# Kernel optimization log

Hardware: AMD Instinct MI355X
Metric: run time of the kernel (lower is better)

Reference implementation:

```python
import jax, jax.numpy as jnp
import numpy as np

D_MODEL = 1024
NUM_HEADS = 16
HEAD_DIM = D_MODEL // NUM_HEADS


def setup_inputs() -> dict:
    key = jax.random.key(0)
    ks = jax.random.split(key, 9)
    s = 1.0 / np.sqrt(D_MODEL)
    def lin(k):
        kw, kb = jax.random.split(k)
        W = jax.random.uniform(kw, (D_MODEL, D_MODEL), jnp.float32, -s, s)
        b = jax.random.uniform(kb, (D_MODEL,), jnp.float32, -s, s)
        return W, b
    Wq, bq = lin(ks[0])
    Wk, bk = lin(ks[1])
    Wv, bv = lin(ks[2])
    Wo, bo = lin(ks[3])
    x = jax.random.normal(ks[4], (4, 2048, D_MODEL), jnp.float32)
    return {"x": x, "Wq": Wq, "bq": bq, "Wk": Wk, "bk": bk,
            "Wv": Wv, "bv": bv, "Wo": Wo, "bo": bo}


def reference(x, Wq, bq, Wk, bk, Wv, bv, Wo, bo):
    B, S, _ = x.shape
    def heads(W, b):
        # [B,S,D] -> [B,H,S,Dh]
        return (x @ W.T + b).reshape(B, S, NUM_HEADS, HEAD_DIM).transpose(0, 2, 1, 3)
    q = heads(Wq, bq)
    k = heads(Wk, bk)
    v = heads(Wv, bv)
    scale = jnp.sqrt(jnp.float32(HEAD_DIM))
    scores = jnp.einsum('bhqd,bhkd->bhqk', q, k) / scale  # [B,H,S,S]
    attn = jax.nn.softmax(scores, axis=-1)
    ctx = jnp.einsum('bhqk,bhkd->bhqd', attn, v)
    ctx = ctx.transpose(0, 2, 1, 3).reshape(B, S, D_MODEL)
    out = ctx @ Wo.T + bo
    return out
```

## Files before the change

### kernel.cpp

```cpp
#include <hip/hip_runtime.h>
#include <hip/hip_bf16.h>

typedef __bf16 bf16;
typedef __attribute__((ext_vector_type(4))) __bf16 bf16x4;
typedef __attribute__((ext_vector_type(8))) __bf16 bf16x8;
typedef __attribute__((ext_vector_type(4))) float floatx4;

#define MFMA_16x16x32(a, b, c) __builtin_amdgcn_mfma_f32_16x16x32_bf16((a), (b), (c), 0, 0, 0)

#define SOFTMAX_SC 0.18033688011112042f

__device__ __forceinline__ void async_lds16(const bf16* g, bf16* lds) {
  __builtin_amdgcn_global_load_lds(
      (__attribute__((address_space(1))) void*)(g),
      (__attribute__((address_space(3))) void*)(lds),
      16, 0, 0);
}

__global__ __launch_bounds__(256) void cast_all_kernel(
    const float* __restrict__ x,
    const float* __restrict__ Wq, const float* __restrict__ Wk,
    const float* __restrict__ Wv, const float* __restrict__ Wo,
    bf16* __restrict__ dst)
{
  const size_t xN = (size_t)8192 * 1024;
  size_t i = ((size_t)blockIdx.x * 256 + threadIdx.x) * 8;
  const float* src;
  size_t off;
  if (i < xN) { src = x; off = i; }
  else {
    size_t j = i - xN;
    int w = (int)(j >> 20);
    off = j & (((size_t)1 << 20) - 1);
    src = (w == 0) ? Wq : (w == 1) ? Wk : (w == 2) ? Wv : Wo;
  }
  floatx4 a = *(const floatx4*)(src + off);
  floatx4 b = *(const floatx4*)(src + off + 4);
  bf16x8 r;
  r[0] = (bf16)a[0]; r[1] = (bf16)a[1]; r[2] = (bf16)a[2]; r[3] = (bf16)a[3];
  r[4] = (bf16)b[0]; r[5] = (bf16)b[1]; r[6] = (bf16)b[2]; r[7] = (bf16)b[3];
  *(bf16x8*)(dst + i) = r;
}

template <typename CT>
__device__ __forceinline__ void gemm128_async_body(
    const bf16* __restrict__ A, const bf16* __restrict__ W,
    const float* __restrict__ bias, CT* __restrict__ C)
{
  __shared__ __align__(16) bf16 As[128 * 64];
  __shared__ __align__(16) bf16 Bs[128 * 64];

  const int tid  = threadIdx.x;
  const int lane = tid & 63;
  const int wave = tid >> 6;
  const int quad = lane >> 4;
  const int l15  = lane & 15;

  const int gm0   = blockIdx.y * 128;
  const int gn0   = blockIdx.x * 128;
  const int m_off = (wave >> 1) * 64;
  const int n_off = (wave & 1) * 64;

  floatx4 acc[4][4] = {};

  const bf16* ap[4];
  const bf16* wp[4];
  #pragma unroll
  for (int i = 0; i < 4; ++i) {
    int c = i * 256 + tid;
    int srow = c >> 3;
    int ksw  = (c & 7) ^ (srow & 7);
    ap[i] = A + (size_t)(gm0 + srow) * 1024 + ksw * 8;
    wp[i] = W + (size_t)(gn0 + srow) * 1024 + ksw * 8;
  }

  for (int kt = 0; kt < 16; ++kt) {
    __syncthreads();
    #pragma unroll
    for (int i = 0; i < 4; ++i) {
      int c = i * 256 + tid;
      async_lds16(ap[i], &As[c * 8]);
      async_lds16(wp[i], &Bs[c * 8]);
      ap[i] += 64; wp[i] += 64;
    }
    __syncthreads();

    #pragma unroll
    for (int kk = 0; kk < 2; ++kk) {
      bf16x8 af[4], bfr[4];
      #pragma unroll
      for (int i = 0; i < 4; ++i) {
        int rm = m_off + i * 16 + l15;
        af[i]  = *(const bf16x8*)&As[rm * 64 + (((kk * 4 + quad) ^ (rm & 7)) * 8)];
        int rn = n_off + i * 16 + l15;
        bfr[i] = *(const bf16x8*)&Bs[rn * 64 + (((kk * 4 + quad) ^ (rn & 7)) * 8)];
      }
      #pragma unroll
      for (int i = 0; i < 4; ++i)
        #pragma unroll
        for (int j = 0; j < 4; ++j)
          acc[i][j] = MFMA_16x16x32(af[i], bfr[j], acc[i][j]);
    }
  }

  #pragma unroll
  for (int j = 0; j < 4; ++j) {
    const int gcol = gn0 + n_off + j * 16 + l15;
    const float bv = bias[gcol];
    #pragma unroll
    for (int i = 0; i < 4; ++i) {
      const int gr = gm0 + m_off + i * 16 + quad * 4;
      #pragma unroll
      for (int r = 0; r < 4; ++r)
        C[(size_t)(gr + r) * 1024 + gcol] = (CT)(acc[i][j][r] + bv);
    }
  }
}

__global__ __launch_bounds__(256) void o_gemm_async(
    const bf16* __restrict__ ctx, const bf16* __restrict__ Wob,
    const float* __restrict__ bo, float* __restrict__ out)
{
  gemm128_async_body<float>(ctx, Wob, bo, out);
}

__global__ __launch_bounds__(512, 4) void qkv_gemm256(
    const bf16* __restrict__ xb,
    const bf16* __restrict__ Wqb, const float* __restrict__ bq,
    const bf16* __restrict__ Wkb, const float* __restrict__ bk,
    const bf16* __restrict__ Wvb, const float* __restrict__ bv,
    bf16* Q, bf16* K, bf16* Vt)
{
  __shared__ __align__(16) bf16 As[256 * 64];
  __shared__ __align__(16) bf16 Bs[128 * 64];

  const int z = blockIdx.z;
  const bf16* W = (z == 0) ? Wqb : (z == 1) ? Wkb : Wvb;
  const float* bias = (z == 0) ? bq : (z == 1) ? bk : bv;

  const int tid  = threadIdx.x;
  const int lane = tid & 63;
  const int wave = tid >> 6;
  const int quad = lane >> 4;
  const int l15  = lane & 15;

  const int gm0   = blockIdx.y * 256;
  const int gn0   = blockIdx.x * 128;
  const int m_off = (wave >> 1) * 64;
  const int n_off = (wave & 1) * 64;

  floatx4 acc[4][4] = {};

  const bf16* ap[4];
  const bf16* wp[2];
  #pragma unroll
  for (int i = 0; i < 4; ++i) {
    int c = i * 512 + tid;
    int srow = c >> 3;
    int ksw  = (c & 7) ^ (srow & 7);
    ap[i] = xb + (size_t)(gm0 + srow) * 1024 + ksw * 8;
  }
  #pragma unroll
  for (int i = 0; i < 2; ++i) {
    int c = i * 512 + tid;
    int srow = c >> 3;
    int ksw  = (c & 7) ^ (srow & 7);
    wp[i] = W + (size_t)(gn0 + srow) * 1024 + ksw * 8;
  }

  for (int kt = 0; kt < 16; ++kt) {
    __syncthreads();
    #pragma unroll
    for (int i = 0; i < 4; ++i) {
      async_lds16(ap[i], &As[(i * 512 + tid) * 8]);
      ap[i] += 64;
    }
    #pragma unroll
    for (int i = 0; i < 2; ++i) {
      async_lds16(wp[i], &Bs[(i * 512 + tid) * 8]);
      wp[i] += 64;
    }
    __syncthreads();

    #pragma unroll
    for (int kk = 0; kk < 2; ++kk) {
      bf16x8 af[4], bfr[4];
      #pragma unroll
      for (int i = 0; i < 4; ++i) {
        int rm = m_off + i * 16 + l15;
        af[i]  = *(const bf16x8*)&As[rm * 64 + (((kk * 4 + quad) ^ (rm & 7)) * 8)];
        int rn = n_off + i * 16 + l15;
        bfr[i] = *(const bf16x8*)&Bs[rn * 64 + (((kk * 4 + quad) ^ (rn & 7)) * 8)];
      }
      #pragma unroll
      for (int i = 0; i < 4; ++i)
        #pragma unroll
        for (int j = 0; j < 4; ++j)
          acc[i][j] = MFMA_16x16x32(af[i], bfr[j], acc[i][j]);
    }
  }

  #pragma unroll
  for (int j = 0; j < 4; ++j) {
    const int gcol = gn0 + n_off + j * 16 + l15;
    const float bv = bias[gcol];
    #pragma unroll
    for (int i = 0; i < 4; ++i) {
      const int gr = gm0 + m_off + i * 16 + quad * 4;
      if (z == 2) {
        const int h  = gcol >> 6;
        const int dh = gcol & 63;
        const size_t base =
            (((size_t)(gr >> 11) * 16 + h) * 64 + dh) * 2048 + (gr & 2047);
        bf16x4 pk;
        #pragma unroll
        for (int r = 0; r < 4; ++r) pk[r] = (bf16)(acc[i][j][r] + bv);
        *(bf16x4*)&Vt[base] = pk;
      } else {
        bf16* dst = (z == 0) ? Q : K;
        const float sc = (z == 0) ? SOFTMAX_SC : 1.0f;
        #pragma unroll
        for (int r = 0; r < 4; ++r)
          dst[(size_t)(gr + r) * 1024 + gcol] = (bf16)((acc[i][j][r] + bv) * sc);
      }
    }
  }
}

__global__ __launch_bounds__(512, 4) void flash6_kernel(
    const bf16* __restrict__ Q, const bf16* __restrict__ Kg,
    const bf16* __restrict__ Vtg, bf16* __restrict__ ctx)
{
  __shared__ __align__(16) bf16 Ks[64 * 64];
  __shared__ __align__(16) bf16 Vts[64 * 64];
  __shared__ __align__(16) bf16 Ps[8 * 32 * 72];

  const int tid  = threadIdx.x;
  const int lane = tid & 63;
  const int wave = tid >> 6;
  const int quad = lane >> 4;
  const int l15  = lane & 15;

  const int bh = blockIdx.y;
  const int b  = bh >> 4;
  const int h  = bh & 15;
  const int qt = blockIdx.x;

  const size_t row0 = (size_t)b * 2048;
  const int col0 = h * 64;

  const int qbase = qt * 256 + wave * 32;
  bf16x8 qf[2][2];
  #pragma unroll
  for (int q = 0; q < 2; ++q) {
    const bf16* qp = Q + (row0 + qbase + q * 16 + l15) * 1024 + col0 + quad * 8;
    qf[q][0] = *(const bf16x8*)(qp);
    qf[q][1] = *(const bf16x8*)(qp + 32);
  }

  floatx4 o_acc[2][4] = {};
  float l_part[2][4] = {};

  const int srow = tid >> 3;
  const int cell = (tid & 7) ^ (srow & 7);
  const bf16* kp = Kg + (row0 + srow) * 1024 + col0 + cell * 8;
  const bf16* vp = Vtg + ((size_t)bh * 64 + srow) * 2048 + cell * 8;
  bf16* const ksd = &Ks[tid * 8];
  bf16* const vtd = &Vts[tid * 8];

  for (int kb = 0; kb < 32; ++kb) {
    __syncthreads();
    async_lds16(kp, ksd);
    async_lds16(vp, vtd);
    kp += 64 * 1024;
    vp += 64;
    __syncthreads();

    #pragma unroll
    for (int j = 0; j < 4; ++j) {
      int rk = j * 16 + l15;
      bf16x8 k0 = *(const bf16x8*)&Ks[rk * 64 + ((quad ^ (rk & 7)) * 8)];
      bf16x8 k1 = *(const bf16x8*)&Ks[rk * 64 + (((4 + quad) ^ (rk & 7)) * 8)];
      #pragma unroll
      for (int q = 0; q < 2; ++q) {
        floatx4 z = {};
        z = MFMA_16x16x32(qf[q][0], k0, z);
        z = MFMA_16x16x32(qf[q][1], k1, z);
        #pragma unroll
        for (int r = 0; r < 4; ++r) {
          float p = exp2f(z[r]);
          l_part[q][r] += p;
          Ps[(wave * 32 + q * 16 + quad * 4 + r) * 72 + j * 16 + l15] = (bf16)p;
        }
      }
    }

    #pragma unroll
    for (int kk = 0; kk < 2; ++kk) {
      bf16x8 vf[4];
      #pragma unroll
      for (int t = 0; t < 4; ++t) {
        int rd = t * 16 + l15;
        vf[t] = *(const bf16x8*)&Vts[rd * 64 + (((kk * 4 + quad) ^ (rd & 7)) * 8)];
      }
      #pragma unroll
      for (int q = 0; q < 2; ++q) {
        bf16x8 pf = *(const bf16x8*)&Ps[(wave * 32 + q * 16 + l15) * 72 + kk * 32 + quad * 8];
        #pragma unroll
        for (int t = 0; t < 4; ++t)
          o_acc[q][t] = MFMA_16x16x32(pf, vf[t], o_acc[q][t]);
      }
    }
  }

  #pragma unroll
  for (int q = 0; q < 2; ++q) {
    #pragma unroll
    for (int off = 1; off < 16; off <<= 1)
      #pragma unroll
      for (int r = 0; r < 4; ++r)
        l_part[q][r] += __shfl_xor(l_part[q][r], off, 64);
    #pragma unroll
    for (int r = 0; r < 4; ++r) l_part[q][r] = 1.0f / l_part[q][r];
    #pragma unroll
    for (int t = 0; t < 4; ++t)
      #pragma unroll
      for (int r = 0; r < 4; ++r) {
        int srow2 = qbase + q * 16 + quad * 4 + r;
        ctx[(row0 + srow2) * 1024 + col0 + t * 16 + l15] =
            (bf16)(o_acc[q][t][r] * l_part[q][r]);
      }
  }
}

__device__ __forceinline__ bf16x8 load8(const bf16* p) { return *(const bf16x8*)p; }
__device__ __forceinline__ bf16x8 load8(const float* p) {
  floatx4 a = *(const floatx4*)p;
  floatx4 b = *(const floatx4*)(p + 4);
  bf16x8 r;
  r[0] = (bf16)a[0]; r[1] = (bf16)a[1]; r[2] = (bf16)a[2]; r[3] = (bf16)a[3];
  r[4] = (bf16)b[0]; r[5] = (bf16)b[1]; r[6] = (bf16)b[2]; r[7] = (bf16)b[3];
  return r;
}

template <typename AT, typename CT>
__device__ __forceinline__ void gemm128_body_fb(
    const AT* __restrict__ A, const float* __restrict__ W,
    const float* __restrict__ bias, CT* __restrict__ C)
{
  constexpr int LDP = 72;
  __shared__ __align__(16) bf16 As[128 * LDP];
  __shared__ __align__(16) bf16 Bs[128 * LDP];
  const int tid = threadIdx.x, lane = tid & 63, wave = tid >> 6;
  const int quad = lane >> 4, l15 = lane & 15;
  const int gm0 = blockIdx.y * 128, gn0 = blockIdx.x * 128;
  const int m_off = (wave >> 1) * 64, n_off = (wave & 1) * 64;
  floatx4 acc[4][4] = {};
  int srow[4], scol[4];
  #pragma unroll
  for (int i = 0; i < 4; ++i) {
    int c = i * 256 + tid;
    srow[i] = c >> 3; scol[i] = (c & 7) * 8;
  }
  for (int kt = 0; kt < 16; ++kt) {
    bf16x8 ar[4], br[4];
    #pragma unroll
    for (int i = 0; i < 4; ++i) {
      ar[i] = load8(A + (size_t)(gm0 + srow[i]) * 1024 + kt * 64 + scol[i]);
      br[i] = load8(W + (size_t)(gn0 + srow[i]) * 1024 + kt * 64 + scol[i]);
    }
    __syncthreads();
    #pragma unroll
    for (int i = 0; i < 4; ++i) {
      *(bf16x8*)&As[srow[i] * LDP + scol[i]] = ar[i];
      *(bf16x8*)&Bs[srow[i] * LDP + scol[i]] = br[i];
    }
    __syncthreads();
    #pragma unroll
    for (int kk = 0; kk < 2; ++kk) {
      bf16x8 af[4], bfr[4];
      #pragma unroll
      for (int i = 0; i < 4; ++i) {
        af[i]  = *(const bf16x8*)&As[(m_off + i * 16 + l15) * LDP + (kk * 4 + quad) * 8];
        bfr[i] = *(const bf16x8*)&Bs[(n_off + i * 16 + l15) * LDP + (kk * 4 + quad) * 8];
      }
      #pragma unroll
      for (int i = 0; i < 4; ++i)
        #pragma unroll
        for (int j = 0; j < 4; ++j)
          acc[i][j] = MFMA_16x16x32(af[i], bfr[j], acc[i][j]);
    }
  }
  #pragma unroll
  for (int j = 0; j < 4; ++j) {
    const int gcol = gn0 + n_off + j * 16 + l15;
    const float bv = bias[gcol];
    #pragma unroll
    for (int i = 0; i < 4; ++i) {
      const int gr = gm0 + m_off + i * 16 + quad * 4;
      #pragma unroll
      for (int r = 0; r < 4; ++r)
        C[(size_t)(gr + r) * 1024 + gcol] = (CT)(acc[i][j][r] + bv);
    }
  }
}

__global__ __launch_bounds__(256) void qkv_gemm_fb(
    const float* __restrict__ x,
    const float* __restrict__ Wq, const float* __restrict__ bq,
    const float* __restrict__ Wk, const float* __restrict__ bk,
    const float* __restrict__ Wv, const float* __restrict__ bv,
    bf16* Q, bf16* K, bf16* V)
{
  const float* W; const float* bias; bf16* out;
  if (blockIdx.z == 0)      { W = Wq; bias = bq; out = Q; }
  else if (blockIdx.z == 1) { W = Wk; bias = bk; out = K; }
  else                      { W = Wv; bias = bv; out = V; }
  gemm128_body_fb<float, bf16>(x, W, bias, out);
}

__global__ __launch_bounds__(256) void out_gemm_fb(
    const bf16* __restrict__ ctx, const float* __restrict__ Wo,
    const float* __restrict__ bo, float* __restrict__ out)
{
  gemm128_body_fb<bf16, float>(ctx, Wo, bo, out);
}

__global__ __launch_bounds__(512) void flash_fb(
    const bf16* Q, const bf16* __restrict__ Kg, const bf16* __restrict__ Vg,
    bf16* ctx)
{
  __shared__ __align__(16) bf16 Ks[64 * 72];
  __shared__ __align__(16) bf16 Vs[64 * 72];
  __shared__ __align__(16) bf16 Vt[64 * 72];
  __shared__ __align__(16) bf16 Ps[8 * 16 * 72];
  const int tid = threadIdx.x, lane = tid & 63, wave = tid >> 6;
  const int quad = lane >> 4, l15 = lane & 15;
  const int bh = blockIdx.y, b = bh >> 4, h = bh & 15, qt = blockIdx.x;
  const size_t row0 = (size_t)b * 2048;
  const int col0 = h * 64;
  const int qs = qt * 128 + wave * 16 + l15;
  const bf16* qp = Q + (row0 + qs) * 1024 + col0 + quad * 8;
  const bf16x8 qf0 = *(const bf16x8*)(qp);
  const bf16x8 qf1 = *(const bf16x8*)(qp + 32);
  floatx4 o_acc[4] = {};
  float l_part[4] = {0.0f, 0.0f, 0.0f, 0.0f};
  const float SC = SOFTMAX_SC;
  const int srow = tid >> 3, scol = (tid & 7) * 8;
  const bf16* kptr = Kg + (row0 + srow) * 1024 + col0 + scol;
  const bf16* vptr = Vg + (row0 + srow) * 1024 + col0 + scol;
  const int td = tid & 63, tg = tid >> 6;
  for (int kb = 0; kb < 32; ++kb) {
    bf16x8 kr = *(const bf16x8*)kptr;
    bf16x8 vr = *(const bf16x8*)vptr;
    kptr += 64 * 1024; vptr += 64 * 1024;
    __syncthreads();
    *(bf16x8*)&Ks[srow * 72 + scol] = kr;
    *(bf16x8*)&Vs[srow * 72 + scol] = vr;
    __syncthreads();
    {
      bf16x8 t;
      #pragma unroll
      for (int j = 0; j < 8; ++j) t[j] = Vs[(tg * 8 + j) * 72 + td];
      *(bf16x8*)&Vt[td * 72 + tg * 8] = t;
    }
    floatx4 sc[4];
    #pragma unroll
    for (int j = 0; j < 4; ++j) {
      int rk = j * 16 + l15;
      bf16x8 k0 = *(const bf16x8*)&Ks[rk * 72 + quad * 8];
      bf16x8 k1 = *(const bf16x8*)&Ks[rk * 72 + 32 + quad * 8];
      floatx4 z = {};
      z = MFMA_16x16x32(qf0, k0, z);
      z = MFMA_16x16x32(qf1, k1, z);
      sc[j] = z;
    }
    #pragma unroll
    for (int j = 0; j < 4; ++j)
      #pragma unroll
      for (int r = 0; r < 4; ++r) {
        float p = exp2f(fminf(sc[j][r] * SC, 60.0f));
        sc[j][r] = p;
        l_part[r] += p;
      }
    #pragma unroll
    for (int j = 0; j < 4; ++j)
      #pragma unroll
      for (int r = 0; r < 4; ++r)
        Ps[(wave * 16 + quad * 4 + r) * 72 + j * 16 + l15] = (bf16)sc[j][r];
    __syncthreads();
    #pragma unroll
    for (int kk = 0; kk < 2; ++kk) {
      bf16x8 pf = *(const bf16x8*)&Ps[(wave * 16 + l15) * 72 + kk * 32 + quad * 8];
      #pragma unroll
      for (int t = 0; t < 4; ++t) {
        bf16x8 vf = *(const bf16x8*)&Vt[(t * 16 + l15) * 72 + kk * 32 + quad * 8];
        o_acc[t] = MFMA_16x16x32(pf, vf, o_acc[t]);
      }
    }
  }
  #pragma unroll
  for (int off = 1; off < 16; off <<= 1)
    #pragma unroll
    for (int r = 0; r < 4; ++r)
      l_part[r] += __shfl_xor(l_part[r], off, 64);
  #pragma unroll
  for (int r = 0; r < 4; ++r) l_part[r] = 1.0f / l_part[r];
  #pragma unroll
  for (int t = 0; t < 4; ++t)
    #pragma unroll
    for (int r = 0; r < 4; ++r) {
      int srow2 = qt * 128 + wave * 16 + quad * 4 + r;
      ctx[(row0 + srow2) * 1024 + col0 + t * 16 + l15] = (bf16)(o_acc[t][r] * l_part[r]);
    }
}

extern "C" void kernel_launch(void* const* d_in, const int* in_sizes, int n_in,
                              void* d_out, int out_size, void* d_ws, size_t ws_size,
                              hipStream_t stream) {
  (void)in_sizes; (void)n_in; (void)out_size;
  const float* x  = (const float*)d_in[0];
  const float* Wq = (const float*)d_in[1];
  const float* bq = (const float*)d_in[2];
  const float* Wk = (const float*)d_in[3];
  const float* bk = (const float*)d_in[4];
  const float* Wv = (const float*)d_in[5];
  const float* bv = (const float*)d_in[6];
  const float* Wo = (const float*)d_in[7];
  const float* bo = (const float*)d_in[8];
  float* out = (float*)d_out;

  const size_t nE = (size_t)8192 * 1024;
  const size_t wE = (size_t)1024 * 1024;
  const size_t need = (5 * nE + 4 * wE) * sizeof(bf16);

  if (ws_size >= need) {
    bf16* Qw   = (bf16*)d_ws;
    bf16* Kw   = Qw + nE;
    bf16* Vtw  = Kw + nE;
    bf16* ctxw = Vtw + nE;
    bf16* xb   = ctxw + nE;
    bf16* Wqb  = xb + nE;
    bf16* Wkb  = Wqb + wE;
    bf16* Wvb  = Wkb + wE;
    bf16* Wob  = Wvb + wE;

    cast_all_kernel<<<dim3(6144), 256, 0, stream>>>(x, Wq, Wk, Wv, Wo, xb);

    qkv_gemm256<<<dim3(8, 32, 3), 512, 0, stream>>>(
        xb, Wqb, bq, Wkb, bk, Wvb, bv, Qw, Kw, Vtw);
    flash6_kernel<<<dim3(8, 64), 512, 0, stream>>>(Qw, Kw, Vtw, ctxw);
    o_gemm_async<<<dim3(8, 64), 256, 0, stream>>>(ctxw, Wob, bo, out);
  } else {
    bf16* Qw = (bf16*)d_ws;
    bf16* Kw = Qw + nE;
    bf16* Vw = Kw + nE;
    bf16* ctx = (ws_size >= 4 * nE * sizeof(bf16)) ? (Vw + nE) : Qw;
    qkv_gemm_fb<<<dim3(8, 64, 3), 256, 0, stream>>>(x, Wq, bq, Wk, bk, Wv, bv, Qw, Kw, Vw);
    flash_fb<<<dim3(16, 64), 512, 0, stream>>>(Qw, Kw, Vw, ctx);
    out_gemm_fb<<<dim3(8, 64), 256, 0, stream>>>(ctx, Wo, bo, out);
  }
}
```

Before: 305.6 us.

## Double-buffer K/V tiles in flash kernel and transpose score MFMA for vector P stores

The flash attention kernel now double-buffers the K and V^T tiles in LDS. It prefetches the next tile right after a single barrier per iteration, so the global-to-LDS copy overlaps compute and one barrier per iteration goes away. The QK^T MFMA operands are swapped so each lane holds four key scores for one query row. That allows packed bf16x4 stores of P and a cheaper row-sum reduction: a local add plus two cross-quad shuffles instead of a 16-lane butterfly. The PV MFMAs are raised in priority with s_setprio. The cost is double the K/V LDS footprint, which may cut occupancy.

```diff
diff --git a/kernel.cpp b/kernel.cpp
--- a/kernel.cpp
+++ b/kernel.cpp
@@ -227,12 +227,12 @@
   }
 }
 
-__global__ __launch_bounds__(512, 4) void flash6_kernel(
+__global__ __launch_bounds__(512, 4) void flash7_kernel(
     const bf16* __restrict__ Q, const bf16* __restrict__ Kg,
     const bf16* __restrict__ Vtg, bf16* __restrict__ ctx)
 {
-  __shared__ __align__(16) bf16 Ks[64 * 64];
-  __shared__ __align__(16) bf16 Vts[64 * 64];
+  __shared__ __align__(16) bf16 Ks[2][64 * 64];
+  __shared__ __align__(16) bf16 Vts[2][64 * 64];
   __shared__ __align__(16) bf16 Ps[8 * 32 * 72];
 
   const int tid  = threadIdx.x;
@@ -259,39 +259,54 @@
   }
 
   floatx4 o_acc[2][4] = {};
-  float l_part[2][4] = {};
+  float l_sum[2] = {0.0f, 0.0f};
 
   const int srow = tid >> 3;
   const int cell = (tid & 7) ^ (srow & 7);
   const bf16* kp = Kg + (row0 + srow) * 1024 + col0 + cell * 8;
   const bf16* vp = Vtg + ((size_t)bh * 64 + srow) * 2048 + cell * 8;
-  bf16* const ksd = &Ks[tid * 8];
-  bf16* const vtd = &Vts[tid * 8];
+  const int soff = tid * 8;
+
+  async_lds16(kp, &Ks[0][soff]);
+  async_lds16(vp, &Vts[0][soff]);
+  kp += 64 * 1024;
+  vp += 64;
+
+  bf16* const ps_base = &Ps[(wave * 32 + l15) * 72];
 
   for (int kb = 0; kb < 32; ++kb) {
-    __syncthreads();
-    async_lds16(kp, ksd);
-    async_lds16(vp, vtd);
-    kp += 64 * 1024;
-    vp += 64;
-    __syncthreads();
+    const int cur = kb & 1;
+    const bf16* const Kc = Ks[cur];
+    const bf16* const Vc = Vts[cur];
+
+    __syncthreads();
+
+    if (kb < 31) {
+      async_lds16(kp, &Ks[cur ^ 1][soff]);
+      async_lds16(vp, &Vts[cur ^ 1][soff]);
+      kp += 64 * 1024;
+      vp += 64;
+    }
 
     #pragma unroll
     for (int j = 0; j < 4; ++j) {
-      int rk = j * 16 + l15;
-      bf16x8 k0 = *(const bf16x8*)&Ks[rk * 64 + ((quad ^ (rk & 7)) * 8)];
-      bf16x8 k1 = *(const bf16x8*)&Ks[rk * 64 + (((4 + quad) ^ (rk & 7)) * 8)];
+      const int rk = j * 16 + l15;
+      bf16x8 k0 = *(const bf16x8*)&Kc[rk * 64 + ((quad ^ (rk & 7)) * 8)];
+      bf16x8 k1 = *(const bf16x8*)&Kc[rk * 64 + (((4 + quad) ^ (rk & 7)) * 8)];
       #pragma unroll
       for (int q = 0; q < 2; ++q) {
         floatx4 z = {};
-        z = MFMA_16x16x32(qf[q][0], k0, z);
-        z = MFMA_16x16x32(qf[q][1], k1, z);
+        z = MFMA_16x16x32(k0, qf[q][0], z);
+        z = MFMA_16x16x32(k1, qf[q][1], z);
+        bf16x4 pk;
         #pragma unroll
         for (int r = 0; r < 4; ++r) {
           float p = exp2f(z[r]);
-          l_part[q][r] += p;
-          Ps[(wave * 32 + q * 16 + quad * 4 + r) * 72 + j * 16 + l15] = (bf16)p;
+          z[r] = p;
+          pk[r] = (bf16)p;
         }
+        l_sum[q] += (z[0] + z[1]) + (z[2] + z[3]);
+        *(bf16x4*)(ps_base + q * (16 * 72) + j * 16 + quad * 4) = pk;
       }
     }
 
@@ -300,36 +315,41 @@
       bf16x8 vf[4];
       #pragma unroll
       for (int t = 0; t < 4; ++t) {
-        int rd = t * 16 + l15;
-        vf[t] = *(const bf16x8*)&Vts[rd * 64 + (((kk * 4 + quad) ^ (rd & 7)) * 8)];
-      }
-      #pragma unroll
-      for (int q = 0; q < 2; ++q) {
-        bf16x8 pf = *(const bf16x8*)&Ps[(wave * 32 + q * 16 + l15) * 72 + kk * 32 + quad * 8];
-        #pragma unroll
-        for (int t = 0; t < 4; ++t)
-          o_acc[q][t] = MFMA_16x16x32(pf, vf[t], o_acc[q][t]);
-      }
+        const int rd = t * 16 + l15;
+        vf[t] = *(const bf16x8*)&Vc[rd * 64 + (((kk * 4 + quad) ^ (rd & 7)) * 8)];
+      }
+      bf16x8 pf0 = *(const bf16x8*)(ps_base + kk * 32 + quad * 8);
+      bf16x8 pf1 = *(const bf16x8*)(ps_base + 16 * 72 + kk * 32 + quad * 8);
+      __builtin_amdgcn_s_setprio(1);
+      #pragma unroll
+      for (int t = 0; t < 4; ++t) {
+        o_acc[0][t] = MFMA_16x16x32(pf0, vf[t], o_acc[0][t]);
+        o_acc[1][t] = MFMA_16x16x32(pf1, vf[t], o_acc[1][t]);
+      }
+      __builtin_amdgcn_s_setprio(0);
     }
   }
 
   #pragma unroll
   for (int q = 0; q < 2; ++q) {
-    #pragma unroll
-    for (int off = 1; off < 16; off <<= 1)
-      #pragma unroll
-      for (int r = 0; r < 4; ++r)
-        l_part[q][r] += __shfl_xor(l_part[q][r], off, 64);
-    #pragma unroll
-    for (int r = 0; r < 4; ++r) l_part[q][r] = 1.0f / l_part[q][r];
-    #pragma unroll
-    for (int t = 0; t < 4; ++t)
+    l_sum[q] += __shfl_xor(l_sum[q], 16, 64);
+    l_sum[q] += __shfl_xor(l_sum[q], 32, 64);
+  }
+  #pragma unroll
+  for (int q = 0; q < 2; ++q) {
+    float li[4];
+    #pragma unroll
+    for (int r = 0; r < 4; ++r)
+      li[r] = 1.0f / __shfl(l_sum[q], quad * 4 + r, 64);
+    #pragma unroll
+    for (int t = 0; t < 4; ++t) {
+      const int gc = col0 + t * 16 + l15;
       #pragma unroll
       for (int r = 0; r < 4; ++r) {
-        int srow2 = qbase + q * 16 + quad * 4 + r;
-        ctx[(row0 + srow2) * 1024 + col0 + t * 16 + l15] =
-            (bf16)(o_acc[q][t][r] * l_part[q][r]);
-      }
+        const int srow2 = qbase + q * 16 + quad * 4 + r;
+        ctx[(row0 + srow2) * 1024 + gc] = (bf16)(o_acc[q][t][r] * li[r]);
+      }
+    }
   }
 }
 
@@ -549,7 +569,7 @@
 
     qkv_gemm256<<<dim3(8, 32, 3), 512, 0, stream>>>(
         xb, Wqb, bq, Wkb, bk, Wvb, bv, Qw, Kw, Vtw);
-    flash6_kernel<<<dim3(8, 64), 512, 0, stream>>>(Qw, Kw, Vtw, ctxw);
+    flash7_kernel<<<dim3(8, 64), 512, 0, stream>>>(Qw, Kw, Vtw, ctxw);
     o_gemm_async<<<dim3(8, 64), 256, 0, stream>>>(ctxw, Wob, bo, out);
   } else {
     bf16* Qw = (bf16*)d_ws;
```

Measured after the change: 307.8 us. Within noise of the previous version (+0.7%).
